# Optimization experiments

Measured on AMD Instinct MI355X. Metric: run time of the kernel, lower is better.

The kernel has to match this reference:

```python
import jax, jax.numpy as jnp
import numpy as np

B, C, H, W = 4, 64, 160, 160
K = 3
KK = K * K
PAD = (K - 1) // 2
EPS = 1e-5


def conv2d(x, w, b):
    y = jax.lax.conv_general_dilated(
        x, w, (1, 1), [(PAD, PAD), (PAD, PAD)],
        dimension_numbers=('NCHW', 'OIHW', 'NCHW'))
    return y + b[None, :, None, None]


def batchnorm(x, g, b, m, v):
    # eval-mode BN with running stats
    return (x - m[None, :, None, None]) * jax.lax.rsqrt(v + EPS)[None, :, None, None] * g[None, :, None, None] + b[None, :, None, None]


def bilinear_gather(x, py, px):
    # x: [B,C,H,W]; py,px: [B,KK,H,W] float sample coords -> [B,C,KK,H,W]
    Bx, Cx, Hx, Wx = x.shape
    y0 = jnp.floor(py)
    x0 = jnp.floor(px)
    ly = py - y0
    lx = px - x0
    x_flat = x.reshape(Bx, Cx, 1, Hx * Wx)
    acc = jnp.zeros((Bx, Cx, py.shape[1], Hx * Wx), dtype=x.dtype)
    corners = ((y0, x0, (1 - ly) * (1 - lx)),
               (y0, x0 + 1, (1 - ly) * lx),
               (y0 + 1, x0, ly * (1 - lx)),
               (y0 + 1, x0 + 1, ly * lx))
    for yi, xi, wgt in corners:
        valid = (yi >= 0) & (yi < Hx) & (xi >= 0) & (xi < Wx)
        yc = jnp.clip(yi, 0, Hx - 1).astype(jnp.int32)
        xc = jnp.clip(xi, 0, Wx - 1).astype(jnp.int32)
        idx = (yc * Wx + xc).reshape(Bx, -1, Hx * Wx)          # [B,KK,HW]
        g = jnp.take_along_axis(x_flat, idx[:, None], axis=3)  # [B,C,KK,HW]
        acc = acc + (wgt * valid).reshape(Bx, 1, -1, Hx * Wx) * g
    return acc.reshape(Bx, Cx, -1, Hx, Wx)


def modulated_deform_conv(x, offset, mask, weight):
    # x:[B,C,H,W] offset:[B,2*KK,H,W] (mmcv layout: pairs (dy,dx) interleaved) mask:[B,KK,H,W]
    Bx, Cx, Hx, Wx = x.shape
    Co = weight.shape[0]
    off = offset.reshape(Bx, KK, 2, Hx, Wx)
    k = jnp.arange(KK)
    ki = (k // K).astype(x.dtype)
    kj = (k % K).astype(x.dtype)
    ys = jnp.arange(Hx, dtype=x.dtype)
    xs = jnp.arange(Wx, dtype=x.dtype)
    py = ys[None, None, :, None] - PAD + ki[None, :, None, None] + off[:, :, 0]
    px = xs[None, None, None, :] - PAD + kj[None, :, None, None] + off[:, :, 1]
    samp = bilinear_gather(x, py, px)            # [B,C,KK,H,W]
    samp = samp * mask[:, None]                  # modulation
    return jnp.einsum('bckhw,ock->bohw', samp, weight.reshape(Co, Cx, KK))


def setup_inputs() -> dict:
    key = jax.random.key(0)
    ks = jax.random.split(key, 16)
    inp = {
        'x': jax.random.normal(ks[0], (B, C, H, W), jnp.float32),
        'w_om1': jax.random.normal(ks[1], (3 * KK, C, K, K), jnp.float32) * 0.01,
        'b_om1': jax.random.normal(ks[2], (3 * KK,), jnp.float32) * 0.01,
        'w_dcn1': jax.random.normal(ks[3], (C, C, K, K), jnp.float32) * 0.04,
        'bn1_g': jax.random.uniform(ks[4], (C,), jnp.float32, 0.5, 1.5),
        'bn1_b': jax.random.normal(ks[5], (C,), jnp.float32) * 0.1,
        'bn1_m': jax.random.normal(ks[6], (C,), jnp.float32) * 0.1,
        'bn1_v': jax.random.uniform(ks[7], (C,), jnp.float32, 0.5, 1.5),
        'w_om2': jax.random.normal(ks[8], (3 * KK, C, K, K), jnp.float32) * 0.01,
        'b_om2': jax.random.normal(ks[9], (3 * KK,), jnp.float32) * 0.01,
        'w_dcn2': jax.random.normal(ks[10], (C, C, K, K), jnp.float32) * 0.04,
        'bn2_g': jax.random.uniform(ks[11], (C,), jnp.float32, 0.5, 1.5),
        'bn2_b': jax.random.normal(ks[12], (C,), jnp.float32) * 0.1,
        'bn2_m': jax.random.normal(ks[13], (C,), jnp.float32) * 0.1,
        'bn2_v': jax.random.uniform(ks[14], (C,), jnp.float32, 0.5, 1.5),
    }
    return inp


def reference(x, w_om1, b_om1, w_dcn1, bn1_g, bn1_b, bn1_m, bn1_v,
              w_om2, b_om2, w_dcn2, bn2_g, bn2_b, bn2_m, bn2_v):
    identity = x
    om1 = conv2d(x, w_om1, b_om1)
    o1, o2, m1 = jnp.split(om1, 3, axis=1)
    offset1 = jnp.concatenate([o1, o2], axis=1)
    mask1 = jax.nn.sigmoid(m1)
    out = modulated_deform_conv(x, offset1, mask1, w_dcn1)
    out = batchnorm(out, bn1_g, bn1_b, bn1_m, bn1_v)
    out = jax.nn.gelu(out, approximate=False)
    om2 = conv2d(out, w_om2, b_om2)
    o1b, o2b, m2 = jnp.split(om2, 3, axis=1)
    offset2 = jnp.concatenate([o1b, o2b], axis=1)
    mask2 = jax.nn.sigmoid(m2)
    out = modulated_deform_conv(out, offset2, mask2, w_dcn2)
    out = batchnorm(out, bn2_g, bn2_b, bn2_m, bn2_v)
    out = out + identity
    return jax.nn.gelu(out, approximate=False)
```

## Files before the change

### kernel.cpp

```cpp
#include <hip/hip_runtime.h>
#include <math.h>

#define HH 160
#define WW 160
#define HWSZ 25600
#define TR 14
#define TC 22
#define NSLOT 308

typedef __attribute__((ext_vector_type(8))) short short8;
typedef __attribute__((ext_vector_type(4))) short short4v;
typedef __attribute__((ext_vector_type(8))) _Float16 half8;
typedef __attribute__((ext_vector_type(2))) _Float16 half2v;
typedef __attribute__((ext_vector_type(4))) float f32x4;
typedef __attribute__((ext_vector_type(16))) float f32x16;
typedef __attribute__((ext_vector_type(2))) unsigned int uint2v;

__device__ __forceinline__ short f2h(float f) {
  union { _Float16 h; short s; } u; u.h = (_Float16)f; return u.s;
}
__device__ __forceinline__ float h2f(short s) {
  union { _Float16 h; short s; } u; u.s = s; return (float)u.h;
}
__device__ __forceinline__ half2v bcast_h(short s) {
  unsigned int x = (unsigned short)s; x |= x << 16;
  union { unsigned int u; half2v h; } v; v.u = x; return v.h;
}

__global__ __launch_bounds__(256) void pre_kernel(
    const float* __restrict__ x,
    const float* __restrict__ g1, const float* __restrict__ b1,
    const float* __restrict__ m1, const float* __restrict__ v1,
    const float* __restrict__ g2, const float* __restrict__ b2,
    const float* __restrict__ m2, const float* __restrict__ v2,
    const float* __restrict__ wd1, const float* __restrict__ wd2,
    const float* __restrict__ wo1, const float* __restrict__ wo2,
    float* __restrict__ sc, short* __restrict__ wd1h, short* __restrict__ wd2h,
    short* __restrict__ wo1h, short* __restrict__ wo2h,
    short* __restrict__ xcl) {
  __shared__ short tmp[64][72];
  int t = threadIdx.x;
  int bx = blockIdx.x;
  if (bx < 1600) {
    int b = bx / 400, p0 = (bx - b * 400) * 64;
    const float* xb = x + (size_t)b * 64 * HWSZ;
    for (int i = t; i < 4096; i += 256) {
      int c = i >> 6, p = i & 63;
      tmp[p][c] = f2h(xb[c * HWSZ + p0 + p]);
    }
    __syncthreads();
    short* ob = xcl + ((size_t)b * HWSZ + p0) * 64;
    for (int i = t; i < 512; i += 256) {
      int p = i >> 3, g = i & 7;
      *(short8*)&ob[p * 64 + g * 8] = *(const short8*)&tmp[p][g * 8];
    }
    return;
  }
  int i0 = (bx - 1600) * 256 + t;
  for (int i = i0; i < 36864; i += 16384) {
    int j = i & 7, oc = (i >> 3) & 31, hi = (i >> 8) & 1;
    int ot = (i >> 9) & 1, s = (i >> 10) & 3, tap = i >> 12;
    int src = (ot * 32 + oc) * 576 + (s * 16 + hi * 8 + j) * 9 + tap;
    wd1h[i] = f2h(wd1[src]);
    wd2h[i] = f2h(wd2[src]);
  }
  for (int i = i0; i < 18432; i += 16384) {
    int j = i & 7, oc = (i >> 3) & 31, hi = (i >> 8) & 1;
    int s = (i >> 9) & 3, tap = i >> 11;
    int src = oc * 576 + (s * 16 + hi * 8 + j) * 9 + tap;
    wo1h[i] = (oc < 27) ? f2h(wo1[src]) : (short)0;
    wo2h[i] = (oc < 27) ? f2h(wo2[src]) : (short)0;
  }
  if (i0 < 64) {
    float s1 = g1[i0] * rsqrtf(v1[i0] + 1e-5f);
    sc[i0]       = s1;
    sc[64 + i0]  = b1[i0] - m1[i0] * s1;
    float s2 = g2[i0] * rsqrtf(v2[i0] + 1e-5f);
    sc[128 + i0] = s2;
    sc[192 + i0] = b2[i0] - m2[i0] * s2;
  }
}

__global__ __launch_bounds__(256, 4) void dcn_fused(
    const short* __restrict__ xcl,
    const short* __restrict__ who,
    const float* __restrict__ bias_om,
    const short* __restrict__ whd,
    const float* __restrict__ scale, const float* __restrict__ shift,
    const short* __restrict__ id_cl,
    short* __restrict__ out_cl,
    float* __restrict__ out_f32) {
  __shared__ short xt[NSLOT * 64];

  int t = threadIdx.x;
  int x0 = blockIdx.x * 16, y0 = blockIdx.y * 8, b = blockIdx.z;
  int w = t >> 6, lane = t & 63, m = lane & 15;
  int hi = lane >> 5, p31 = lane & 31;
  int ybase = y0 - 3, xbase = x0 - 3;

  const short* xb = xcl + (size_t)b * HWSZ * 64;
  for (int i = t; i < NSLOT * 8; i += 256) {
    int slot = i >> 3, g = i & 7;
    int ty = slot / TC, tx = slot - ty * TC;
    int gy = ybase + ty, gx = xbase + tx;
    short8 v = {};
    if (gy >= 0 && gy < HH && gx >= 0 && gx < WW)
      v = *(const short8*)&xb[(gy * WW + gx) * 64 + g * 8];
    *(short8*)&xt[slot * 64 + ((g ^ (slot & 7)) << 3)] = v;
  }
  __syncthreads();

  union { short s[32]; unsigned int u[16]; } omr;
  {
    f32x16 oacc = {};
#pragma unroll
    for (int k9 = 0; k9 < 9; k9++) {
      int ki = k9 / 3, kj = k9 - ki * 3;
      int slotb = (w * 2 + (p31 >> 4) + ki + 2) * TC + ((p31 & 15) + kj + 2);
#pragma unroll
      for (int s = 0; s < 4; s++) {
        int g = s * 2 + hi;
        union { short8 s8; half8 h; } A, B;
        B.s8 = *(const short8*)&xt[slotb * 64 + ((g ^ (slotb & 7)) << 3)];
        A.s8 = *(const short8*)&who[((k9 * 4 + s) * 64 + lane) * 8];
        oacc = __builtin_amdgcn_mfma_f32_32x32x16_f16(A.h, B.h, oacc, 0, 0, 0);
      }
    }
#pragma unroll
    for (int j = 0; j < 8; j++) {
      int c0 = 2 * (j & 1) + 8 * (j >> 1);
      int oc0 = c0 + 4 * hi;
      float b0 = (oc0 < 27) ? bias_om[oc0] : 0.f;
      float b1 = (oc0 + 1 < 27) ? bias_om[oc0 + 1] : 0.f;
      union { unsigned int u; short s2[2]; } pk;
      pk.s2[0] = f2h(oacc[2 * j] + b0);
      pk.s2[1] = f2h(oacc[2 * j + 1] + b1);
      uint2v sw = __builtin_amdgcn_permlane32_swap(pk.u, pk.u, false, false);
      omr.u[c0 >> 1]       = sw[0];
      omr.u[(c0 + 4) >> 1] = sw[1];
    }
  }

  int y = y0 + w * 2 + (p31 >> 4), x = x0 + m;

  short4v ivs[8];
  if (out_f32) {
    size_t pbase = ((size_t)b * HWSZ + y * WW + x) * 64;
#pragma unroll
    for (int ot = 0; ot < 2; ot++)
#pragma unroll
      for (int blk = 0; blk < 4; blk++)
        ivs[ot * 4 + blk] =
            *(const short4v*)&id_cl[pbase + ot * 32 + blk * 8 + hi * 4];
  }

  f32x16 acc0 = {}, acc1 = {};
#pragma unroll
  for (int k = 0; k < 9; ++k) {
    float dy = h2f(omr.s[2 * k]);
    float dx = h2f(omr.s[2 * k + 1]);
    float ml = h2f(omr.s[18 + k]);
    float msk = 1.f / (1.f + __expf(-ml));
    int ki = k / 3, kj = k - ki * 3;
    float py  = (float)(y - 1 + ki) + dy;
    float pxf = (float)(x - 1 + kj) + dx;
    float fy = floorf(py), fx = floorf(pxf);
    float ly = py - fy, lx = pxf - fx;
    int yi0 = (int)fy, xi0 = (int)fx;
    bool vy0 = (yi0 >= 0) & (yi0 < HH), vy1 = (yi0 + 1 >= 0) & (yi0 + 1 < HH);
    bool vx0 = (xi0 >= 0) & (xi0 < WW), vx1 = (xi0 + 1 >= 0) & (xi0 + 1 < WW);
    int ty0 = min(max(yi0 - ybase, 0), TR - 2);
    int tx0 = min(max(xi0 - xbase, 0), TC - 2);
    int p00 = ty0 * TC + tx0;
    half2v w00 = bcast_h(f2h((vy0 & vx0) ? (1.f - ly) * (1.f - lx) * msk : 0.f));
    half2v w01 = bcast_h(f2h((vy0 & vx1) ? (1.f - ly) * lx * msk : 0.f));
    half2v w10 = bcast_h(f2h((vy1 & vx0) ? ly * (1.f - lx) * msk : 0.f));
    half2v w11 = bcast_h(f2h((vy1 & vx1) ? ly * lx * msk : 0.f));
    int s00 = p00, s01 = p00 + 1, s10 = p00 + TC, s11 = p00 + TC + 1;
#pragma unroll
    for (int s = 0; s < 4; s++) {
      int g = s * 2 + hi;
      union { short8 s8; half2v h[4]; } c00, c01, c10, c11, bb;
      c00.s8 = *(const short8*)&xt[s00 * 64 + ((g ^ (s00 & 7)) << 3)];
      c01.s8 = *(const short8*)&xt[s01 * 64 + ((g ^ (s01 & 7)) << 3)];
      c10.s8 = *(const short8*)&xt[s10 * 64 + ((g ^ (s10 & 7)) << 3)];
      c11.s8 = *(const short8*)&xt[s11 * 64 + ((g ^ (s11 & 7)) << 3)];
#pragma unroll
      for (int d = 0; d < 4; d++)
        bb.h[d] = c00.h[d] * w00 + c01.h[d] * w01 + c10.h[d] * w10 +
                  c11.h[d] * w11;
      const short* ap = whd + k * 4096 + s * 1024 + lane * 8;
      short8 a0 = *(const short8*)ap;
      short8 a1 = *(const short8*)(ap + 512);
      union { short8 s8; half8 h8; } B, A0, A1;
      B.s8 = bb.s8; A0.s8 = a0; A1.s8 = a1;
      acc0 = __builtin_amdgcn_mfma_f32_32x32x16_f16(A0.h8, B.h8, acc0, 0, 0, 0);
      acc1 = __builtin_amdgcn_mfma_f32_32x32x16_f16(A1.h8, B.h8, acc1, 0, 0, 0);
    }
  }

  if (out_f32) {
#pragma unroll
    for (int ot = 0; ot < 2; ot++) {
#pragma unroll
      for (int r = 0; r < 16; r++) {
        int oc = ot * 32 + (r & 3) + 8 * (r >> 2) + 4 * hi;
        float a = ot ? acc1[r] : acc0[r];
        size_t idx = ((size_t)(b * 64 + oc)) * HWSZ + y * WW + x;
        float v = a * scale[oc] + shift[oc] + h2f(ivs[ot * 4 + (r >> 2)][r & 3]);
        v = 0.5f * v * (1.f + erff(v * 0.70710678118654752f));
        out_f32[idx] = v;
      }
    }
  } else {
    size_t base = ((size_t)b * HWSZ + y * WW + x) * 64;
#pragma unroll
    for (int ot = 0; ot < 2; ot++) {
#pragma unroll
      for (int blk = 0; blk < 4; blk++) {
        short4v pv;
#pragma unroll
        for (int rr = 0; rr < 4; rr++) {
          int r = blk * 4 + rr;
          int oc = ot * 32 + blk * 8 + hi * 4 + rr;
          float a = ot ? acc1[r] : acc0[r];
          float v = a * scale[oc] + shift[oc];
          v = 0.5f * v * (1.f + erff(v * 0.70710678118654752f));
          pv[rr] = f2h(v);
        }
        *(short4v*)&out_cl[base + ot * 32 + blk * 8 + hi * 4] = pv;
      }
    }
  }
}

extern "C" void kernel_launch(void* const* d_in, const int* in_sizes, int n_in,
                              void* d_out, int out_size, void* d_ws, size_t ws_size,
                              hipStream_t stream) {
  const float* x     = (const float*)d_in[0];
  const float* w_om1 = (const float*)d_in[1];
  const float* b_om1 = (const float*)d_in[2];
  const float* w_d1  = (const float*)d_in[3];
  const float* bn1g  = (const float*)d_in[4];
  const float* bn1b  = (const float*)d_in[5];
  const float* bn1m  = (const float*)d_in[6];
  const float* bn1v  = (const float*)d_in[7];
  const float* w_om2 = (const float*)d_in[8];
  const float* b_om2 = (const float*)d_in[9];
  const float* w_d2  = (const float*)d_in[10];
  const float* bn2g  = (const float*)d_in[11];
  const float* bn2b  = (const float*)d_in[12];
  const float* bn2m  = (const float*)d_in[13];
  const float* bn2v  = (const float*)d_in[14];

  float* ws    = (float*)d_ws;
  float* sc    = ws;
  short* w1h   = (short*)(ws + 256);
  short* w2h   = w1h + 36864;
  short* wo1h  = w2h + 36864;
  short* wo2h  = wo1h + 18432;
  short* x_cl  = (short*)(ws + 55552);
  short* o1_cl = x_cl + 6553600;
  float* outp  = (float*)d_out;

  pre_kernel<<<dim3(1664), dim3(256), 0, stream>>>(
      x, bn1g, bn1b, bn1m, bn1v, bn2g, bn2b, bn2m, bn2v,
      w_d1, w_d2, w_om1, w_om2, sc, w1h, w2h, wo1h, wo2h, x_cl);

  dim3 grid(WW / 16, HH / 8, 4);
  dcn_fused<<<grid, dim3(256), 0, stream>>>(
      x_cl, wo1h, b_om1, w1h, sc, sc + 64, nullptr, o1_cl, nullptr);
  dcn_fused<<<grid, dim3(256), 0, stream>>>(
      o1_cl, wo2h, b_om2, w2h, sc + 128, sc + 192, x_cl, nullptr, outp);
}
```

Baseline: 183.2 us.

## Software-pipeline deformable gather and weight loads, precompute bilinear weights

Precomputes bilinear corner weights and tile base indices for all 9 taps up front, then runs a flattened 36-step loop. Each step prefetches the next step's LDS corner values and global weight fragments into double buffers while the current step blends and issues MFMAs. The identity-residual loads move after the main loop, and launch bounds drop to 3 blocks per CU to leave room for the extra registers. This is meant to hide LDS and global load latency behind MFMA work, at the cost of higher register pressure and lower occupancy.

```diff
diff --git a/kernel.cpp b/kernel.cpp
--- a/kernel.cpp
+++ b/kernel.cpp
@@ -81,7 +81,7 @@
   }
 }
 
-__global__ __launch_bounds__(256, 4) void dcn_fused(
+__global__ __launch_bounds__(256, 3) void dcn_fused(
     const short* __restrict__ xcl,
     const short* __restrict__ who,
     const float* __restrict__ bias_om,
@@ -143,18 +143,8 @@
 
   int y = y0 + w * 2 + (p31 >> 4), x = x0 + m;
 
-  short4v ivs[8];
-  if (out_f32) {
-    size_t pbase = ((size_t)b * HWSZ + y * WW + x) * 64;
-#pragma unroll
-    for (int ot = 0; ot < 2; ot++)
-#pragma unroll
-      for (int blk = 0; blk < 4; blk++)
-        ivs[ot * 4 + blk] =
-            *(const short4v*)&id_cl[pbase + ot * 32 + blk * 8 + hi * 4];
-  }
-
-  f32x16 acc0 = {}, acc1 = {};
+  half2v wgt[9][4];
+  int bs[9];
 #pragma unroll
   for (int k = 0; k < 9; ++k) {
     float dy = h2f(omr.s[2 * k]);
@@ -171,35 +161,69 @@
     bool vx0 = (xi0 >= 0) & (xi0 < WW), vx1 = (xi0 + 1 >= 0) & (xi0 + 1 < WW);
     int ty0 = min(max(yi0 - ybase, 0), TR - 2);
     int tx0 = min(max(xi0 - xbase, 0), TC - 2);
-    int p00 = ty0 * TC + tx0;
-    half2v w00 = bcast_h(f2h((vy0 & vx0) ? (1.f - ly) * (1.f - lx) * msk : 0.f));
-    half2v w01 = bcast_h(f2h((vy0 & vx1) ? (1.f - ly) * lx * msk : 0.f));
-    half2v w10 = bcast_h(f2h((vy1 & vx0) ? ly * (1.f - lx) * msk : 0.f));
-    half2v w11 = bcast_h(f2h((vy1 & vx1) ? ly * lx * msk : 0.f));
-    int s00 = p00, s01 = p00 + 1, s10 = p00 + TC, s11 = p00 + TC + 1;
-#pragma unroll
-    for (int s = 0; s < 4; s++) {
-      int g = s * 2 + hi;
-      union { short8 s8; half2v h[4]; } c00, c01, c10, c11, bb;
-      c00.s8 = *(const short8*)&xt[s00 * 64 + ((g ^ (s00 & 7)) << 3)];
-      c01.s8 = *(const short8*)&xt[s01 * 64 + ((g ^ (s01 & 7)) << 3)];
-      c10.s8 = *(const short8*)&xt[s10 * 64 + ((g ^ (s10 & 7)) << 3)];
-      c11.s8 = *(const short8*)&xt[s11 * 64 + ((g ^ (s11 & 7)) << 3)];
-#pragma unroll
-      for (int d = 0; d < 4; d++)
-        bb.h[d] = c00.h[d] * w00 + c01.h[d] * w01 + c10.h[d] * w10 +
-                  c11.h[d] * w11;
-      const short* ap = whd + k * 4096 + s * 1024 + lane * 8;
-      short8 a0 = *(const short8*)ap;
-      short8 a1 = *(const short8*)(ap + 512);
-      union { short8 s8; half8 h8; } B, A0, A1;
-      B.s8 = bb.s8; A0.s8 = a0; A1.s8 = a1;
-      acc0 = __builtin_amdgcn_mfma_f32_32x32x16_f16(A0.h8, B.h8, acc0, 0, 0, 0);
-      acc1 = __builtin_amdgcn_mfma_f32_32x32x16_f16(A1.h8, B.h8, acc1, 0, 0, 0);
-    }
-  }
+    bs[k] = ty0 * TC + tx0;
+    wgt[k][0] = bcast_h(f2h((vy0 & vx0) ? (1.f - ly) * (1.f - lx) * msk : 0.f));
+    wgt[k][1] = bcast_h(f2h((vy0 & vx1) ? (1.f - ly) * lx * msk : 0.f));
+    wgt[k][2] = bcast_h(f2h((vy1 & vx0) ? ly * (1.f - lx) * msk : 0.f));
+    wgt[k][3] = bcast_h(f2h((vy1 & vx1) ? ly * lx * msk : 0.f));
+  }
+
+#define CLOAD(dst, kk, ss)                                                   \
+  do {                                                                       \
+    int g_ = (ss) * 2 + hi;                                                  \
+    int p_ = bs[kk];                                                         \
+    dst[0] = *(const short8*)&xt[p_ * 64 + ((g_ ^ (p_ & 7)) << 3)];          \
+    dst[1] = *(const short8*)&xt[(p_ + 1) * 64 +                             \
+                                 ((g_ ^ ((p_ + 1) & 7)) << 3)];              \
+    dst[2] = *(const short8*)&xt[(p_ + TC) * 64 +                            \
+                                 ((g_ ^ ((p_ + TC) & 7)) << 3)];             \
+    dst[3] = *(const short8*)&xt[(p_ + TC + 1) * 64 +                        \
+                                 ((g_ ^ ((p_ + TC + 1) & 7)) << 3)];         \
+  } while (0)
+
+  f32x16 acc0 = {}, acc1 = {};
+  short8 cor[2][4];
+  short8 pa0, pa1;
+  CLOAD(cor[0], 0, 0);
+  pa0 = *(const short8*)&whd[lane * 8];
+  pa1 = *(const short8*)&whd[512 + lane * 8];
+#pragma unroll
+  for (int i = 0; i < 36; ++i) {
+    int k = i >> 2;
+    int cur = i & 1;
+    if (i + 1 < 36) {
+      int nk = (i + 1) >> 2, ns = (i + 1) & 3;
+      CLOAD(cor[cur ^ 1], nk, ns);
+    }
+    short8 A0 = pa0, A1 = pa1;
+    if (i + 1 < 36) {
+      int nk = (i + 1) >> 2, ns = (i + 1) & 3;
+      pa0 = *(const short8*)&whd[nk * 4096 + ns * 1024 + lane * 8];
+      pa1 = *(const short8*)&whd[nk * 4096 + ns * 1024 + 512 + lane * 8];
+    }
+    union { short8 s8; half2v h[4]; } c0, c1, c2, c3, bb;
+    c0.s8 = cor[cur][0]; c1.s8 = cor[cur][1];
+    c2.s8 = cor[cur][2]; c3.s8 = cor[cur][3];
+#pragma unroll
+    for (int d = 0; d < 4; d++)
+      bb.h[d] = c0.h[d] * wgt[k][0] + c1.h[d] * wgt[k][1] +
+                c2.h[d] * wgt[k][2] + c3.h[d] * wgt[k][3];
+    union { short8 s8; half8 h8; } B, UA0, UA1;
+    B.s8 = bb.s8; UA0.s8 = A0; UA1.s8 = A1;
+    acc0 = __builtin_amdgcn_mfma_f32_32x32x16_f16(UA0.h8, B.h8, acc0, 0, 0, 0);
+    acc1 = __builtin_amdgcn_mfma_f32_32x32x16_f16(UA1.h8, B.h8, acc1, 0, 0, 0);
+  }
+#undef CLOAD
 
   if (out_f32) {
+    short4v ivs[8];
+    size_t pbase = ((size_t)b * HWSZ + y * WW + x) * 64;
+#pragma unroll
+    for (int ot = 0; ot < 2; ot++)
+#pragma unroll
+      for (int blk = 0; blk < 4; blk++)
+        ivs[ot * 4 + blk] =
+            *(const short4v*)&id_cl[pbase + ot * 32 + blk * 8 + hi * 4];
 #pragma unroll
     for (int ot = 0; ot < 2; ot++) {
 #pragma unroll
```

Measured after the change: 189.1 us. +3.2%, slower.
